# Optimization experiments

Hardware: AMD Instinct MI355X
Metric: run time of the kernel (lower is better)

The kernel has to match this reference:

```python
import jax, jax.numpy as jnp
import numpy as np

N, D, P, NS = 2048, 64, 32, 512  # nnodes, stop_embedding_size, preference_dim, n_active_stops
LEAKY_SLOPE = 0.01
COS_EPS = 1e-8


def setup_inputs() -> dict:
    key = jax.random.key(0)
    ks = jax.random.split(key, 10)
    dist = jax.random.uniform(ks[0], (N, N), dtype=jnp.float32)
    stops = jax.random.randint(ks[1], (NS,), 0, N)
    emb_w = jax.random.normal(ks[2], (N, D), dtype=jnp.float32) * 0.05      # nn.Embedding weight
    lin_l_w = jax.random.normal(ks[3], (P, D), dtype=jnp.float32) * 0.05    # SAGEConv lin_l (aggregated)
    lin_l_b = jnp.zeros((P,), dtype=jnp.float32)
    lin_r_w = jax.random.normal(ks[4], (P, D), dtype=jnp.float32) * 0.05    # SAGEConv lin_r (root)
    edge_w = jax.random.normal(ks[5], (2 * P,), dtype=jnp.float32) * 0.05   # edge_summarizer weight
    edge_b = jnp.zeros((), dtype=jnp.float32)
    in_len = 2 * N + 3 + P
    comb_w = jax.random.normal(ks[6], (N, in_len), dtype=jnp.float32) * 0.02  # combiner weight
    comb_b = jnp.zeros((N,), dtype=jnp.float32)
    return {
        "dist": dist, "emb_w": emb_w,
        "lin_l_w": lin_l_w, "lin_l_b": lin_l_b, "lin_r_w": lin_r_w,
        "edge_w": edge_w, "edge_b": edge_b,
        "comb_w": comb_w, "comb_b": comb_b,
        "stops": stops, "weekday": 3, "vehicles": 5,
    }


def reference(dist, emb_w, lin_l_w, lin_l_b, lin_r_w, edge_w, edge_b,
              comb_w, comb_b, stops, weekday, vehicles):
    dt = emb_w.dtype
    # --- cosine-similarity graph build ---
    norm = jnp.maximum(jnp.linalg.norm(emb_w, axis=1, keepdims=True), COS_EPS)
    xn = emb_w / norm
    sim = xn @ xn.T                                   # [N, N]
    sim = sim * (1.0 - jnp.eye(N, dtype=dt))          # fill_diagonal_(0)
    keep = jnp.zeros((N,), dtype=bool).at[stops].set(True)
    adj = ((sim > 0.5) & keep[:, None] & keep[None, :]).astype(dt)  # [N, N]
    # --- SAGEConv (mean aggregation): lin_l(mean_j x_j) + lin_r(x_i) ---
    deg = jnp.maximum(adj.sum(axis=1, keepdims=True), 1.0)
    agg = (adj @ emb_w) / deg                         # [N, D]
    pref = agg @ lin_l_w.T + lin_l_b + emb_w @ lin_r_w.T   # [N, P]
    # --- all-pairs edge summaries: Linear([pref_i, pref_j]) + LeakyReLU ---
    # equivalent to concat-then-linear, without materializing [N^2, 2P]
    a = pref @ edge_w[:P]                             # [N]
    b = pref @ edge_w[P:]                             # [N]
    es = a[:, None] + b[None, :] + edge_b             # [N, N]
    es = jnp.where(es >= 0, es, LEAKY_SLOPE * es)
    # --- combiner + log-softmax ---
    weekday_feat = jnp.full((N, 1), weekday, dtype=dt)
    vehicle_feat = jnp.full((N, 1), vehicles, dtype=dt)
    stop_feat = keep.astype(dt)[:, None]
    combined = jnp.concatenate([pref, es, dist, weekday_feat, vehicle_feat, stop_feat], axis=1)
    out = combined @ comb_w.T + comb_b                # [N, N]
    return jax.nn.log_softmax(out, axis=1)
```

## Files before the change

### kernel.cpp

```cpp
#include <hip/hip_runtime.h>

typedef unsigned short u16;
typedef __attribute__((ext_vector_type(8))) short bf16x8;
typedef __attribute__((ext_vector_type(4))) float f32x4;

__device__ __forceinline__ u16 f2bf(float f) {
    return (u16)((__float_as_uint(f) + 0x8000u) >> 16);
}

#define N_NODES 2048
#define D_EMB 64
#define P_DIM 32
#define NS_STOPS 512
#define IN_LEN 4131
#define NKT 65

#define SWZ(row, c) ((((row) * 8) + ((c) ^ ((row) & 7))) * 8)

__device__ __forceinline__ void gload16(const u16* g, u16* l) {
    __builtin_amdgcn_global_load_lds((const __attribute__((address_space(1))) void*)g,
                                     (__attribute__((address_space(3))) void*)l, 16, 0, 0);
}

__global__ __launch_bounds__(256) void k_aggpref(const float* __restrict__ emb, const int* __restrict__ stops,
                                                 const float* __restrict__ lin_l_w, const float* __restrict__ lin_l_b,
                                                 const float* __restrict__ lin_r_w, const float* __restrict__ edge_w,
                                                 float* __restrict__ pref, float* __restrict__ av, float* __restrict__ bv) {
    int i = blockIdx.x, t = threadIdx.x;
    __shared__ int bm[64];
    __shared__ int kl[NS_STOPS];
    __shared__ int cnt, degL;
    __shared__ float xi[D_EMB];
    __shared__ float aggL[D_EMB];
    __shared__ float niS;
    if (t < 64) bm[t] = 0;
    if (t == 0) { cnt = 0; degL = 0; }
    if (t < D_EMB) { xi[t] = emb[i * D_EMB + t]; aggL[t] = 0.f; }
    __syncthreads();
    {
        int s0 = stops[t], s1 = stops[t + 256];
        atomicOr(&bm[s0 >> 5], 1 << (s0 & 31));
        atomicOr(&bm[s1 >> 5], 1 << (s1 & 31));
    }
    __syncthreads();
    {
        int w = bm[t >> 2];
        int base = (t >> 2) * 32 + (t & 3) * 8;
        #pragma unroll
        for (int e = 0; e < 8; ++e)
            if ((w >> ((t & 3) * 8 + e)) & 1) { int p = atomicAdd(&cnt, 1); kl[p] = base + e; }
    }
    if (t < 64) {
        float s = xi[t] * xi[t];
        #pragma unroll
        for (int off = 32; off; off >>= 1) s += __shfl_xor(s, off, 64);
        if (t == 0) niS = fmaxf(sqrtf(s), 1e-8f);
    }
    __syncthreads();
    int ki = (bm[i >> 5] >> (i & 31)) & 1;
    if (ki) {
        int nk = cnt;
        float ni = niS;
        const f32x4* xiv = (const f32x4*)xi;
        for (int u = t; u < nk; u += 256) {
            int j = kl[u];
            if (j == i) continue;
            const f32x4* ej = (const f32x4*)&emb[j * D_EMB];
            f32x4 er[16];
            f32x4 dv = {0.f, 0.f, 0.f, 0.f};
            f32x4 sv = {0.f, 0.f, 0.f, 0.f};
            #pragma unroll
            for (int d = 0; d < 16; ++d) {
                er[d] = ej[d];
                dv += xiv[d] * er[d];
                sv += er[d] * er[d];
            }
            float dot = dv[0] + dv[1] + dv[2] + dv[3];
            float nj = fmaxf(sqrtf(sv[0] + sv[1] + sv[2] + sv[3]), 1e-8f);
            if (dot > 0.5f * ni * nj) {
                atomicAdd(&degL, 1);
                #pragma unroll
                for (int d = 0; d < 16; ++d) {
                    atomicAdd(&aggL[d * 4 + 0], er[d][0]);
                    atomicAdd(&aggL[d * 4 + 1], er[d][1]);
                    atomicAdd(&aggL[d * 4 + 2], er[d][2]);
                    atomicAdd(&aggL[d * 4 + 3], er[d][3]);
                }
            }
        }
    }
    __syncthreads();
    if (t < D_EMB) {
        float deg = fmaxf((float)degL, 1.0f);
        aggL[t] = ki ? (aggL[t] / deg) : 0.f;
    }
    __syncthreads();
    if (t < P_DIM) {
        float s = lin_l_b[t];
        const float* wl = &lin_l_w[t * D_EMB];
        const float* wr = &lin_r_w[t * D_EMB];
        #pragma unroll
        for (int d = 0; d < D_EMB; ++d) s += aggL[d] * wl[d] + xi[d] * wr[d];
        pref[i * P_DIM + t] = s;
        float a = s * edge_w[t];
        float b = s * edge_w[P_DIM + t];
        #pragma unroll
        for (int off = 16; off; off >>= 1) { a += __shfl_xor(a, off, 64); b += __shfl_xor(b, off, 64); }
        if (t == 0) { av[i] = a; bv[i] = b; }
    }
}

__global__ __launch_bounds__(256) void k_pack(const float* __restrict__ comb_w, const float* __restrict__ comb_b,
                                              const int* __restrict__ wk_p, const int* __restrict__ vh_p,
                                              const float* __restrict__ dist, const float* __restrict__ pref,
                                              const float* __restrict__ av, const float* __restrict__ bv,
                                              const float* __restrict__ edge_b,
                                              u16* __restrict__ Bp, u16* __restrict__ Ap,
                                              float* __restrict__ cvec, float* __restrict__ w3) {
    int kt = blockIdx.x;
    int ty = blockIdx.y;
    int t = threadIdx.x;
    if (ty < 16) {
        int nt = ty;
        u16* tb = Bp + ((size_t)nt * NKT + kt) * 8192;
        #pragma unroll
        for (int it = 0; it < 4; ++it) {
            int q = t + it * 256;
            int r = q >> 3, c = q & 7;
            int j = nt * 128 + r;
            int k0 = kt * 64 + c * 8;
            const float* cw = comb_w + (size_t)j * IN_LEN;
            bf16x8 v;
            if (k0 < 4096) {
                f32x4 f0, f1;
                __builtin_memcpy(&f0, cw + 32 + k0, 16);
                __builtin_memcpy(&f1, cw + 36 + k0, 16);
                #pragma unroll
                for (int e = 0; e < 4; ++e) { v[e] = (short)f2bf(f0[e]); v[4 + e] = (short)f2bf(f1[e]); }
            } else if (k0 < 4128) {
                f32x4 f0, f1;
                __builtin_memcpy(&f0, cw + (k0 - 4096), 16);
                __builtin_memcpy(&f1, cw + (k0 - 4092), 16);
                #pragma unroll
                for (int e = 0; e < 4; ++e) { v[e] = (short)f2bf(f0[e]); v[4 + e] = (short)f2bf(f1[e]); }
            } else {
                #pragma unroll
                for (int e = 0; e < 8; ++e) v[e] = 0;
            }
            *(bf16x8*)&tb[r * 64 + ((c ^ (r & 7)) * 8)] = v;
        }
        if (kt == 64 && t < 128) {
            int j = nt * 128 + t;
            const float* cw = comb_w + (size_t)j * IN_LEN;
            float wk = (float)wk_p[0], vh = (float)vh_p[0];
            cvec[j] = wk * cw[4128] + vh * cw[4129] + comb_b[j];
            w3[j] = cw[4130];
        }
    } else {
        int rt = ty - 16;
        u16* ta = Ap + ((size_t)rt * NKT + kt) * 4096;
        float eb = edge_b[0];
        #pragma unroll
        for (int it = 0; it < 2; ++it) {
            int q = t + it * 256;
            int r = q >> 3, c = q & 7;
            int row = rt * 64 + r;
            int k0 = kt * 64 + c * 8;
            bf16x8 v;
            if (k0 < 2048) {
                float ab = av[row] + eb;
                f32x4 f0 = *(const f32x4*)(bv + k0);
                f32x4 f1 = *(const f32x4*)(bv + k0 + 4);
                #pragma unroll
                for (int e = 0; e < 4; ++e) {
                    float s0 = ab + f0[e]; s0 = (s0 >= 0.f) ? s0 : 0.01f * s0;
                    float s1 = ab + f1[e]; s1 = (s1 >= 0.f) ? s1 : 0.01f * s1;
                    v[e] = (short)f2bf(s0); v[4 + e] = (short)f2bf(s1);
                }
            } else if (k0 < 4096) {
                const f32x4* dp = (const f32x4*)(dist + (size_t)row * 2048 + (k0 - 2048));
                f32x4 f0 = dp[0], f1 = dp[1];
                #pragma unroll
                for (int e = 0; e < 4; ++e) { v[e] = (short)f2bf(f0[e]); v[4 + e] = (short)f2bf(f1[e]); }
            } else if (k0 < 4128) {
                const f32x4* pp = (const f32x4*)(pref + (size_t)row * P_DIM + (k0 - 4096));
                f32x4 f0 = pp[0], f1 = pp[1];
                #pragma unroll
                for (int e = 0; e < 4; ++e) { v[e] = (short)f2bf(f0[e]); v[4 + e] = (short)f2bf(f1[e]); }
            } else {
                #pragma unroll
                for (int e = 0; e < 8; ++e) v[e] = 0;
            }
            *(bf16x8*)&ta[r * 64 + ((c ^ (r & 7)) * 8)] = v;
        }
    }
}

__global__ __launch_bounds__(256) void k_gemm_d(const u16* __restrict__ Ap, const u16* __restrict__ Bp,
                                                float* __restrict__ Cout) {
    __shared__ __attribute__((aligned(16))) short As[3][64 * 64];
    __shared__ __attribute__((aligned(16))) short Bs[3][128 * 64];
    int t = threadIdx.x;
    int mt = blockIdx.y, nt = blockIdx.x;
    int tileM = mt * 64, tileN = nt * 128;
    int lane = t & 63;
    int wid = t >> 6;
    int waveM = wid & 1, waveN = wid >> 1;
    int l16 = lane & 15, quad = lane >> 4;

    f32x4 acc[2][4];
    #pragma unroll
    for (int a_ = 0; a_ < 2; ++a_)
        #pragma unroll
        for (int b_ = 0; b_ < 4; ++b_) acc[a_][b_] = (f32x4){0.f, 0.f, 0.f, 0.f};

    const u16* ga = Ap + ((size_t)mt * NKT) * 4096 + t * 8;
    const u16* gb = Bp + ((size_t)nt * NKT) * 8192 + t * 8;

#define ISSUE(ktv, bb) do { \
        const u16* gan = ga + (size_t)(ktv) * 4096; \
        const u16* gbn = gb + (size_t)(ktv) * 8192; \
        u16* ad = (u16*)As[bb] + t * 8; \
        u16* bd = (u16*)Bs[bb] + t * 8; \
        gload16(gan, ad); \
        gload16(gan + 2048, ad + 2048); \
        gload16(gbn, bd); \
        gload16(gbn + 2048, bd + 2048); \
        gload16(gbn + 4096, bd + 4096); \
        gload16(gbn + 6144, bd + 6144); \
    } while (0)

    ISSUE(0, 0);
    ISSUE(1, 1);

    int cur = 0;
    for (int kt = 0; kt < NKT; ++kt) {
        if (kt < NKT - 1) asm volatile("s_waitcnt vmcnt(6)" ::: "memory");
        else              asm volatile("s_waitcnt vmcnt(0)" ::: "memory");
        __builtin_amdgcn_sched_barrier(0);
        __builtin_amdgcn_s_barrier();
        __builtin_amdgcn_sched_barrier(0);
        if (kt + 2 < NKT) {
            int b2 = cur + 2; if (b2 >= 3) b2 -= 3;
            ISSUE(kt + 2, b2);
        }
        const short* Asc = As[cur];
        const short* Bsc = Bs[cur];
        #pragma unroll
        for (int kk = 0; kk < 64; kk += 32) {
            int cbase = kk >> 3;
            bf16x8 af[2], bfr[4];
            #pragma unroll
            for (int mi = 0; mi < 2; ++mi) {
                int row = waveM * 32 + mi * 16 + l16;
                af[mi] = *(const bf16x8*)&Asc[SWZ(row, cbase + quad)];
            }
            #pragma unroll
            for (int ni = 0; ni < 4; ++ni) {
                int row = waveN * 64 + ni * 16 + l16;
                bfr[ni] = *(const bf16x8*)&Bsc[SWZ(row, cbase + quad)];
            }
            #pragma unroll
            for (int mi = 0; mi < 2; ++mi)
                #pragma unroll
                for (int ni = 0; ni < 4; ++ni)
                    acc[mi][ni] = __builtin_amdgcn_mfma_f32_16x16x32_bf16(af[mi], bfr[ni], acc[mi][ni], 0, 0, 0);
        }
        cur = cur + 1; if (cur >= 3) cur = 0;
    }
#undef ISSUE
    #pragma unroll
    for (int mi = 0; mi < 2; ++mi)
        #pragma unroll
        for (int ni = 0; ni < 4; ++ni) {
            int row = tileM + waveM * 32 + mi * 16 + quad * 4;
            int col = tileN + waveN * 64 + ni * 16 + l16;
            float* cp = Cout + (size_t)row * N_NODES + col;
            #pragma unroll
            for (int rr = 0; rr < 4; ++rr) cp[(size_t)rr * N_NODES] = acc[mi][ni][rr];
        }
}

__global__ __launch_bounds__(256) void k_epi(const float* __restrict__ cvec, const float* __restrict__ w3,
                                             const int* __restrict__ stops, float* __restrict__ out) {
    int i = blockIdx.x, t = threadIdx.x;
    __shared__ int bm[64];
    __shared__ float redmax[4], redsum[4];
    if (t < 64) bm[t] = 0;
    __syncthreads();
    {
        int s0 = stops[t], s1 = stops[t + 256];
        atomicOr(&bm[s0 >> 5], 1 << (s0 & 31));
        atomicOr(&bm[s1 >> 5], 1 << (s1 & 31));
    }
    __syncthreads();
    float ki = (float)((bm[i >> 5] >> (i & 31)) & 1);
    f32x4* orow = (f32x4*)(out + (size_t)i * N_NODES);
    const f32x4* cv = (const f32x4*)cvec;
    const f32x4* wv = (const f32x4*)w3;
    f32x4 v0 = orow[t] + cv[t] + ki * wv[t];
    f32x4 v1 = orow[t + 256] + cv[t + 256] + ki * wv[t + 256];
    float vmax = fmaxf(fmaxf(fmaxf(v0[0], v0[1]), fmaxf(v0[2], v0[3])),
                       fmaxf(fmaxf(v1[0], v1[1]), fmaxf(v1[2], v1[3])));
    #pragma unroll
    for (int off = 32; off; off >>= 1) vmax = fmaxf(vmax, __shfl_xor(vmax, off, 64));
    if ((t & 63) == 0) redmax[t >> 6] = vmax;
    __syncthreads();
    vmax = fmaxf(fmaxf(redmax[0], redmax[1]), fmaxf(redmax[2], redmax[3]));
    float se = 0.f;
    #pragma unroll
    for (int e = 0; e < 4; ++e) se += expf(v0[e] - vmax) + expf(v1[e] - vmax);
    #pragma unroll
    for (int off = 32; off; off >>= 1) se += __shfl_xor(se, off, 64);
    if ((t & 63) == 0) redsum[t >> 6] = se;
    __syncthreads();
    se = redsum[0] + redsum[1] + redsum[2] + redsum[3];
    float lz = vmax + logf(se);
    orow[t] = v0 - lz;
    orow[t + 256] = v1 - lz;
}

extern "C" void kernel_launch(void* const* d_in, const int* in_sizes, int n_in,
                              void* d_out, int out_size, void* d_ws, size_t ws_size,
                              hipStream_t stream) {
    const float* dist    = (const float*)d_in[0];
    const float* emb     = (const float*)d_in[1];
    const float* lin_l_w = (const float*)d_in[2];
    const float* lin_l_b = (const float*)d_in[3];
    const float* lin_r_w = (const float*)d_in[4];
    const float* edge_w  = (const float*)d_in[5];
    const float* edge_b  = (const float*)d_in[6];
    const float* comb_w  = (const float*)d_in[7];
    const float* comb_b  = (const float*)d_in[8];
    const int* stops     = (const int*)d_in[9];
    const int* wk        = (const int*)d_in[10];
    const int* vh        = (const int*)d_in[11];

    char* ws = (char*)d_ws;
    float* pref  = (float*)(ws + 0);
    float* av    = (float*)(ws + 262144);
    float* bv    = (float*)(ws + 270336);
    float* cvec  = (float*)(ws + 278528);
    float* w3    = (float*)(ws + 286720);
    u16*   Ap    = (u16*)(ws + 294912);
    u16*   Bp    = (u16*)(ws + 17334272);
    float* out   = (float*)d_out;

    hipLaunchKernelGGL(k_aggpref, dim3(2048),   dim3(256), 0, stream, emb, stops,
                       lin_l_w, lin_l_b, lin_r_w, edge_w, pref, av, bv);
    hipLaunchKernelGGL(k_pack,    dim3(65, 48), dim3(256), 0, stream, comb_w, comb_b, wk, vh,
                       dist, pref, av, bv, edge_b, Bp, Ap, cvec, w3);
    hipLaunchKernelGGL(k_gemm_d,  dim3(16, 32), dim3(256), 0, stream, Ap, Bp, out);
    hipLaunchKernelGGL(k_epi,     dim3(2048),   dim3(256), 0, stream, cvec, w3, stops, out);
}
```

Before: 198.4 us.

## Enlarge GEMM tile to 128x128 with double buffering instead of triple

The main GEMM tile grows from 64x128 to 128x128. Each wave now holds a 4x4 grid of MFMA accumulators, and the grid halves to 256 blocks. The LDS pipeline drops from three buffers with a two-deep prefetch to two buffers with a one-deep prefetch and a plain __syncthreads. The goal is more data reuse per loaded tile and less global/LDS traffic per FLOP. The trade-offs are fewer blocks on a 256-CU device (about one per CU), more registers, and less latency hiding from the shallower prefetch.

Result: slower. 220.6 us (+11.2%).

```diff
diff --git a/kernel.cpp b/kernel.cpp
--- a/kernel.cpp
+++ b/kernel.cpp
@@ -198,61 +198,57 @@
 
 __global__ __launch_bounds__(256) void k_gemm_d(const u16* __restrict__ Ap, const u16* __restrict__ Bp,
                                                 float* __restrict__ Cout) {
-    __shared__ __attribute__((aligned(16))) short As[3][64 * 64];
-    __shared__ __attribute__((aligned(16))) short Bs[3][128 * 64];
+    __shared__ __attribute__((aligned(16))) short As[2][128 * 64];
+    __shared__ __attribute__((aligned(16))) short Bs[2][128 * 64];
     int t = threadIdx.x;
     int mt = blockIdx.y, nt = blockIdx.x;
-    int tileM = mt * 64, tileN = nt * 128;
+    int tileM = mt * 128, tileN = nt * 128;
     int lane = t & 63;
     int wid = t >> 6;
     int waveM = wid & 1, waveN = wid >> 1;
     int l16 = lane & 15, quad = lane >> 4;
 
-    f32x4 acc[2][4];
-    #pragma unroll
-    for (int a_ = 0; a_ < 2; ++a_)
+    f32x4 acc[4][4];
+    #pragma unroll
+    for (int a_ = 0; a_ < 4; ++a_)
         #pragma unroll
         for (int b_ = 0; b_ < 4; ++b_) acc[a_][b_] = (f32x4){0.f, 0.f, 0.f, 0.f};
 
-    const u16* ga = Ap + ((size_t)mt * NKT) * 4096 + t * 8;
-    const u16* gb = Bp + ((size_t)nt * NKT) * 8192 + t * 8;
+    const u16* gA = Ap + ((size_t)(2 * mt) * NKT) * 4096 + t * 8;
+    const size_t strideA = (size_t)NKT * 4096;
+    const u16* gB = Bp + ((size_t)nt * NKT) * 8192 + t * 8;
 
 #define ISSUE(ktv, bb) do { \
-        const u16* gan = ga + (size_t)(ktv) * 4096; \
-        const u16* gbn = gb + (size_t)(ktv) * 8192; \
+        const u16* a0 = gA + (size_t)(ktv) * 4096; \
+        const u16* a1 = a0 + strideA; \
+        const u16* b0 = gB + (size_t)(ktv) * 8192; \
         u16* ad = (u16*)As[bb] + t * 8; \
         u16* bd = (u16*)Bs[bb] + t * 8; \
-        gload16(gan, ad); \
-        gload16(gan + 2048, ad + 2048); \
-        gload16(gbn, bd); \
-        gload16(gbn + 2048, bd + 2048); \
-        gload16(gbn + 4096, bd + 4096); \
-        gload16(gbn + 6144, bd + 6144); \
+        gload16(a0, ad); \
+        gload16(a0 + 2048, ad + 2048); \
+        gload16(a1, ad + 4096); \
+        gload16(a1 + 2048, ad + 6144); \
+        gload16(b0, bd); \
+        gload16(b0 + 2048, bd + 2048); \
+        gload16(b0 + 4096, bd + 4096); \
+        gload16(b0 + 6144, bd + 6144); \
     } while (0)
 
     ISSUE(0, 0);
-    ISSUE(1, 1);
 
     int cur = 0;
     for (int kt = 0; kt < NKT; ++kt) {
-        if (kt < NKT - 1) asm volatile("s_waitcnt vmcnt(6)" ::: "memory");
-        else              asm volatile("s_waitcnt vmcnt(0)" ::: "memory");
-        __builtin_amdgcn_sched_barrier(0);
-        __builtin_amdgcn_s_barrier();
-        __builtin_amdgcn_sched_barrier(0);
-        if (kt + 2 < NKT) {
-            int b2 = cur + 2; if (b2 >= 3) b2 -= 3;
-            ISSUE(kt + 2, b2);
-        }
+        __syncthreads();
+        if (kt + 1 < NKT) ISSUE(kt + 1, cur ^ 1);
         const short* Asc = As[cur];
         const short* Bsc = Bs[cur];
         #pragma unroll
         for (int kk = 0; kk < 64; kk += 32) {
             int cbase = kk >> 3;
-            bf16x8 af[2], bfr[4];
-            #pragma unroll
-            for (int mi = 0; mi < 2; ++mi) {
-                int row = waveM * 32 + mi * 16 + l16;
+            bf16x8 af[4], bfr[4];
+            #pragma unroll
+            for (int mi = 0; mi < 4; ++mi) {
+                int row = waveM * 64 + mi * 16 + l16;
                 af[mi] = *(const bf16x8*)&Asc[SWZ(row, cbase + quad)];
             }
             #pragma unroll
@@ -261,19 +257,19 @@
                 bfr[ni] = *(const bf16x8*)&Bsc[SWZ(row, cbase + quad)];
             }
             #pragma unroll
-            for (int mi = 0; mi < 2; ++mi)
+            for (int mi = 0; mi < 4; ++mi)
                 #pragma unroll
                 for (int ni = 0; ni < 4; ++ni)
                     acc[mi][ni] = __builtin_amdgcn_mfma_f32_16x16x32_bf16(af[mi], bfr[ni], acc[mi][ni], 0, 0, 0);
         }
-        cur = cur + 1; if (cur >= 3) cur = 0;
+        cur ^= 1;
     }
 #undef ISSUE
     #pragma unroll
-    for (int mi = 0; mi < 2; ++mi)
+    for (int mi = 0; mi < 4; ++mi)
         #pragma unroll
         for (int ni = 0; ni < 4; ++ni) {
-            int row = tileM + waveM * 32 + mi * 16 + quad * 4;
+            int row = tileM + waveM * 64 + mi * 16 + quad * 4;
             int col = tileN + waveN * 64 + ni * 16 + l16;
             float* cp = Cout + (size_t)row * N_NODES + col;
             #pragma unroll
@@ -350,6 +346,6 @@
                        lin_l_w, lin_l_b, lin_r_w, edge_w, pref, av, bv);
     hipLaunchKernelGGL(k_pack,    dim3(65, 48), dim3(256), 0, stream, comb_w, comb_b, wk, vh,
                        dist, pref, av, bv, edge_b, Bp, Ap, cvec, w3);
-    hipLaunchKernelGGL(k_gemm_d,  dim3(16, 32), dim3(256), 0, stream, Ap, Bp, out);
+    hipLaunchKernelGGL(k_gemm_d,  dim3(16, 16), dim3(256), 0, stream, Ap, Bp, out);
     hipLaunchKernelGGL(k_epi,     dim3(2048),   dim3(256), 0, stream, cvec, w3, stops, out);
 }
```
